# Kernel optimization log

Hardware: AMD Instinct MI355X
Metric: run time of the kernel (lower is better)

The kernel has to match this reference:

```python
import math
import jax, jax.numpy as jnp
import numpy as np

B, T, D, N = 4, 2048, 1024, 4096  # d_neuron = 4*d_model


def setup_inputs() -> dict:
    key = jax.random.key(0)
    ks = jax.random.split(key, 8)
    s_d = 1.0 / math.sqrt(D)
    s_n = 1.0 / math.sqrt(N)
    return {
        "x": jax.random.normal(ks[0], (B, T, D), jnp.float32),
        "state": jnp.zeros((B, N), jnp.float32),
        "W_main": jax.random.normal(ks[1], (D, N), jnp.float32) * s_d,
        "W_gate": jax.random.normal(ks[2], (D, N), jnp.float32) * s_d,
        "W_mod": jax.random.normal(ks[3], (D, N), jnp.float32) * s_d,
        "W_delta": jax.random.normal(ks[4], (D, N), jnp.float32) * s_d,
        "b_delta": jnp.full((N,), -3.0, jnp.float32),
        "W_out": jax.random.normal(ks[5], (N, D), jnp.float32) * s_n,
        "A_log": jnp.linspace(math.log(0.001), math.log(0.1), N).astype(jnp.float32),
        "sw_logit": jnp.zeros((N,), jnp.float32),  # inv_sigmoid(0.5)
    }


def reference(x, state, W_main, W_gate, W_mod, W_delta, b_delta, W_out, A_log, sw_logit):
    raw = jnp.einsum("btd,dn->btn", x, W_main)            # [B,T,N]
    gate = jax.nn.sigmoid(jnp.einsum("btd,dn->btn", x, W_gate))
    mod = jnp.tanh(jnp.einsum("btd,dn->btn", x, W_mod))
    delta = jax.nn.softplus(jnp.einsum("btd,dn->btn", x, W_delta) + b_delta)
    A = -jnp.exp(A_log)                                    # [N]
    decay = jnp.exp(delta * A)                             # [B,T,N]
    update = (1.0 - decay) * gate * jnp.tanh(raw)

    # linear recurrence h_t = decay_t * h_{t-1} + update_t via associative scan
    def combine(c, n):
        a1, b1 = c
        a2, b2 = n
        return a1 * a2, a2 * b1 + b2

    a_cum, b_cum = jax.lax.associative_scan(combine, (decay, update), axis=1)
    all_states = a_cum * state[:, None, :] + b_cum         # [B,T,N]
    final_state = all_states[:, -1]

    sw = jax.nn.sigmoid(sw_logit)
    mixed = (1.0 - sw) * jax.nn.gelu(raw, approximate=False) + sw * all_states
    output = mixed * (1.0 + mod)                           # dropout=0 (eval)
    output = jnp.einsum("btn,nd->btd", output, W_out)
    return output, final_state
```

## Files before the change

### kernel.cpp

```cpp
#include <hip/hip_runtime.h>
#include <math.h>
#include <stdint.h>

#define BB  4
#define TT  2048
#define DD  1024
#define NNq 4096
#define BT  (BB*TT)
#define NCH 16
#define TCH (TT/NCH)

typedef _Float16 f16;
typedef __attribute__((ext_vector_type(8))) _Float16 half8;
typedef __attribute__((ext_vector_type(4))) float f32x4;

__device__ __forceinline__ float sigmoid_f(float x){ return 1.f/(1.f+__expf(-x)); }
__device__ __forceinline__ float tanh_f(float x){
  float cx = fminf(fmaxf(x,-15.f),15.f);
  float e  = __expf(2.f*cx);
  return (e-1.f)/(e+1.f);
}
__device__ __forceinline__ float softplus_f(float x){
  return (x>15.f)? x : __logf(1.f+__expf(x));
}

__global__ __launch_bounds__(256) void cast_f16_k(const float* __restrict__ src,
                                                  f16* __restrict__ dst){
  size_t i = ((size_t)blockIdx.x*256 + threadIdx.x)*4;
  float4 v = *(const float4*)(src + i);
  union { f16 h[4]; uint2 u; } o;
  o.h[0]=(f16)v.x; o.h[1]=(f16)v.y; o.h[2]=(f16)v.z; o.h[3]=(f16)v.w;
  *(uint2*)(dst + i) = o.u;
}

__global__ __launch_bounds__(256) void transpose_cast_k(const float* __restrict__ src,
                                                        f16* __restrict__ dst,
                                                        int R, int C){
  __shared__ float tile[32][33];
  int c0 = blockIdx.x*32, r0 = blockIdx.y*32;
  int tx = threadIdx.x, ty = threadIdx.y;
  #pragma unroll
  for (int i=0;i<4;i++){ int r = ty + i*8; tile[r][tx] = src[(size_t)(r0+r)*C + c0+tx]; }
  __syncthreads();
  #pragma unroll
  for (int i=0;i<4;i++){ int c = ty + i*8; dst[(size_t)(c0+c)*R + r0+tx] = (f16)tile[tx][c]; }
}

template<int OUT_F32>
__global__ __launch_bounds__(256)
void gemm_bt(const f16* __restrict__ A, int lda,
             const f16* __restrict__ Bt, int ldb,
             void* __restrict__ Cout, int ldc, int K)
{
  __shared__ f16 lsA[128*64];
  __shared__ f16 lsB[128*64];
  const int tid  = threadIdx.x;
  const int lane = tid & 63;
  const int wave = tid >> 6;
  const int wm = wave >> 1, wn = wave & 1;
  const int m0 = blockIdx.y * 128;
  const int n0 = blockIdx.x * 128;

  const f16* Ag = A  + (size_t)m0 * lda;
  const f16* Bg = Bt + (size_t)n0 * ldb;

  f32x4 acc[4][4] = {};

  for (int k0 = 0; k0 < K; k0 += 64) {
    half8 ra[4], rb[4];
    #pragma unroll
    for (int i = 0; i < 4; i++) {
      const int j   = i*256 + tid;
      const int row = j >> 3;
      const int ce  = (j & 7) * 8;
      ra[i] = *(const half8*)(Ag + (size_t)row*lda + k0 + ce);
      rb[i] = *(const half8*)(Bg + (size_t)row*ldb + k0 + ce);
    }
    __syncthreads();
    #pragma unroll
    for (int i = 0; i < 4; i++) {
      const int j = i*256 + tid;
      *(half8*)&lsA[j*8] = ra[i];
      *(half8*)&lsB[j*8] = rb[i];
    }
    __syncthreads();
    #pragma unroll
    for (int ks = 0; ks < 2; ks++) {
      const int kk = ks*32 + (lane>>4)*8;
      half8 af[4], bfr[4];
      #pragma unroll
      for (int mi=0; mi<4; mi++)
        af[mi] = *(const half8*)&lsA[(wm*64 + mi*16 + (lane&15))*64 + kk];
      #pragma unroll
      for (int ni=0; ni<4; ni++)
        bfr[ni] = *(const half8*)&lsB[(wn*64 + ni*16 + (lane&15))*64 + kk];
      #pragma unroll
      for (int mi=0; mi<4; mi++)
        #pragma unroll
        for (int ni=0; ni<4; ni++)
          acc[mi][ni] = __builtin_amdgcn_mfma_f32_16x16x32_f16(af[mi], bfr[ni], acc[mi][ni], 0, 0, 0);
    }
  }

  const int crow = m0 + wm*64 + (lane>>4)*4;
  const int ccol = n0 + wn*64 + (lane&15);
  #pragma unroll
  for (int mi=0; mi<4; mi++)
    #pragma unroll
    for (int ni=0; ni<4; ni++)
      #pragma unroll
      for (int r=0; r<4; r++) {
        size_t idx = (size_t)(crow + mi*16 + r) * ldc + (ccol + ni*16);
        if (OUT_F32) ((float*)Cout)[idx] = acc[mi][ni][r];
        else         ((f16*)Cout)[idx]   = (f16)acc[mi][ni][r];
      }
}

__global__ __launch_bounds__(256) void scan_agg_k(
    const f16* __restrict__ zg, const f16* __restrict__ zr, const f16* __restrict__ zd,
    const float* __restrict__ Alog, const float* __restrict__ bdelta,
    float* __restrict__ AggA, float* __restrict__ AggB, int NC)
{
  const int nb = NC >> 8;
  const int bx = blockIdx.x;
  const int nl = (bx % nb)*256 + threadIdx.x;
  const int c  = (bx / nb) % NCH;
  const int b  = bx / (nb*NCH);
  const float An = -__expf(Alog[nl]);
  const float bd = bdelta[nl];
  float pA = 1.f, pB = 0.f;
  const size_t rbase = (size_t)(b*TT + c*TCH);
  #pragma unroll 4
  for (int t=0; t<TCH; ++t) {
    size_t rr = rbase + t;
    float g  = (float)zg[rr*NC  + nl];
    float r  = (float)zr[rr*NNq + nl];
    float dz = (float)zd[rr*NC  + nl] + bd;
    float d  = __expf(An * softplus_f(dz));
    float u  = (1.f-d) * sigmoid_f(g) * tanh_f(r);
    pA *= d;
    pB = fmaf(d, pB, u);
  }
  size_t o = ((size_t)(b*NCH + c))*NNq + nl;
  AggA[o] = pA;
  AggB[o] = pB;
}

__global__ __launch_bounds__(256) void scan_mid_k(
    const float* __restrict__ AggA, const float* __restrict__ AggB,
    const float* __restrict__ state0, float* __restrict__ sIn,
    float* __restrict__ fstate, int NC)
{
  int gi = blockIdx.x*256 + threadIdx.x;
  int b  = gi / NC, nl = gi % NC;
  float s = state0[(size_t)b*NNq + nl];
  #pragma unroll
  for (int c=0; c<NCH; ++c) {
    size_t o = ((size_t)(b*NCH + c))*NNq + nl;
    sIn[o] = s;
    s = fmaf(AggA[o], s, AggB[o]);
  }
  fstate[(size_t)b*NNq + nl] = s;
}

__global__ __launch_bounds__(256) void scan_apply_k(
    const f16* zr, const f16* __restrict__ zg, const f16* __restrict__ zm,
    const f16* __restrict__ zd,
    const float* __restrict__ Alog, const float* __restrict__ bdelta,
    const float* __restrict__ swl, const float* __restrict__ sIn,
    f16* P, int NC)
{
  const int nb = NC >> 8;
  const int bx = blockIdx.x;
  const int nl = (bx % nb)*256 + threadIdx.x;
  const int c  = (bx / nb) % NCH;
  const int b  = bx / (nb*NCH);
  const float An = -__expf(Alog[nl]);
  const float bd = bdelta[nl];
  const float sw = sigmoid_f(swl[nl]);
  float s = sIn[((size_t)(b*NCH + c))*NNq + nl];
  const size_t rbase = (size_t)(b*TT + c*TCH);
  for (int t=0; t<TCH; ++t) {
    size_t rr = rbase + t;
    float r  = (float)zr[rr*NNq + nl];
    float g  = (float)zg[rr*NC  + nl];
    float m  = (float)zm[rr*NC  + nl];
    float dz = (float)zd[rr*NC  + nl] + bd;
    float d  = __expf(An * softplus_f(dz));
    float u  = (1.f-d) * sigmoid_f(g) * tanh_f(r);
    s = fmaf(d, s, u);
    float gel = 0.5f*r*(1.f+erff(r*0.70710678118654752f));
    float mod = tanh_f(m);
    float op  = ((1.f-sw)*gel + sw*s)*(1.f+mod);
    P[rr*NNq + nl] = (f16)op;
  }
}

extern "C" void kernel_launch(void* const* d_in, const int* in_sizes, int n_in,
                              void* d_out, int out_size, void* d_ws, size_t ws_size,
                              hipStream_t stream)
{
  const float* x      = (const float*)d_in[0];
  const float* state0 = (const float*)d_in[1];
  const float* Wmain  = (const float*)d_in[2];
  const float* Wgate  = (const float*)d_in[3];
  const float* Wmod   = (const float*)d_in[4];
  const float* Wdelta = (const float*)d_in[5];
  const float* bdelta = (const float*)d_in[6];
  const float* Wout   = (const float*)d_in[7];
  const float* Alog   = (const float*)d_in[8];
  const float* swl    = (const float*)d_in[9];

  auto al = [](size_t v)->size_t { return (v + 255) & ~(size_t)255; };
  const size_t sz_xb  = al((size_t)BT*DD*2);
  const size_t sz_wt  = al((size_t)NNq*DD*2);
  const size_t sz_wto = al((size_t)DD*NNq*2);
  const size_t sz_P   = al((size_t)BT*NNq*2);
  const size_t sz_agg = al((size_t)BB*NCH*NNq*4);
  const size_t fixed  = sz_xb + 4*sz_wt + sz_wto + sz_P + 3*sz_agg;

  int NCC = 16;
  {
    const int cand[5] = {1,2,4,8,16};
    for (int i=0;i<5;i++){
      size_t zchunk = al((size_t)BT*(NNq/cand[i])*2);
      if (fixed + 3*zchunk <= ws_size) { NCC = cand[i]; break; }
    }
  }
  const int NC = NNq / NCC;
  const size_t sz_z = al((size_t)BT*NC*2);

  char* ws = (char*)d_ws;
  size_t off = 0;
  auto alloc = [&](size_t bytes)->void* { void* p = ws + off; off += bytes; return p; };
  f16*   xb   = (f16*)alloc(sz_xb);
  f16*   wt0  = (f16*)alloc(sz_wt);
  f16*   wt1  = (f16*)alloc(sz_wt);
  f16*   wt2  = (f16*)alloc(sz_wt);
  f16*   wt3  = (f16*)alloc(sz_wt);
  f16*   wto  = (f16*)alloc(sz_wto);
  f16*   P    = (f16*)alloc(sz_P);
  float* AggA = (float*)alloc(sz_agg);
  float* AggB = (float*)alloc(sz_agg);
  float* sIn  = (float*)alloc(sz_agg);
  f16*   z1   = (f16*)alloc(sz_z);
  f16*   z2   = (f16*)alloc(sz_z);
  f16*   z3   = (f16*)alloc(sz_z);

  float* fstate = (float*)d_out + (size_t)BT*DD;

  cast_f16_k<<<(BT*DD)/1024, 256, 0, stream>>>(x, xb);
  transpose_cast_k<<<dim3(NNq/32, DD/32), dim3(32,8), 0, stream>>>(Wmain,  wt0, DD, NNq);
  transpose_cast_k<<<dim3(NNq/32, DD/32), dim3(32,8), 0, stream>>>(Wgate,  wt1, DD, NNq);
  transpose_cast_k<<<dim3(NNq/32, DD/32), dim3(32,8), 0, stream>>>(Wmod,   wt2, DD, NNq);
  transpose_cast_k<<<dim3(NNq/32, DD/32), dim3(32,8), 0, stream>>>(Wdelta, wt3, DD, NNq);
  transpose_cast_k<<<dim3(DD/32, NNq/32), dim3(32,8), 0, stream>>>(Wout,   wto, NNq, DD);

  const dim3 gz(NC/128, BT/128);
  for (int cc = 0; cc < NCC; ++cc) {
    const int n0 = cc * NC;
    gemm_bt<0><<<gz, 256, 0, stream>>>(xb, DD, wt0 + (size_t)n0*DD, DD, P + n0, NNq, DD);
    gemm_bt<0><<<gz, 256, 0, stream>>>(xb, DD, wt1 + (size_t)n0*DD, DD, z1, NC, DD);
    gemm_bt<0><<<gz, 256, 0, stream>>>(xb, DD, wt2 + (size_t)n0*DD, DD, z2, NC, DD);
    gemm_bt<0><<<gz, 256, 0, stream>>>(xb, DD, wt3 + (size_t)n0*DD, DD, z3, NC, DD);
    scan_agg_k<<<BB*NCH*(NC/256), 256, 0, stream>>>(z1, P + n0, z3,
        Alog + n0, bdelta + n0, AggA + n0, AggB + n0, NC);
    scan_mid_k<<<(BB*NC)/256, 256, 0, stream>>>(AggA + n0, AggB + n0,
        state0 + n0, sIn + n0, fstate + n0, NC);
    scan_apply_k<<<BB*NCH*(NC/256), 256, 0, stream>>>(P + n0, z1, z2, z3,
        Alog + n0, bdelta + n0, swl + n0, sIn + n0, P + n0, NC);
  }

  gemm_bt<1><<<dim3(DD/128, BT/128), 256, 0, stream>>>(P, NNq, wto, NNq, d_out, DD, NNq);
}
```

Baseline: 967.5 us.

## Use direct global-to-LDS loads, XCD-aware tile remap, vectorized scans, more chunks

The GEMM now stages tiles with global_load_lds, which writes straight into shared memory instead of going through registers, and remaps workgroup IDs so neighbouring tiles land on the same XCD for better L2 reuse. The scan aggregate and apply kernels get vectorized variants that have each thread handle 2 or 4 neurons with packed f16 loads and stores. The number of time chunks doubles to raise scan parallelism. The trade-off is that the GEMM loses its register prefetch overlap, since the load now sits between two barriers, and the remap assumes the workgroup count is divisible by 8.

```diff
diff --git a/kernel.cpp b/kernel.cpp
--- a/kernel.cpp
+++ b/kernel.cpp
@@ -7,11 +7,13 @@
 #define DD  1024
 #define NNq 4096
 #define BT  (BB*TT)
-#define NCH 16
+#define NCH 32
 #define TCH (TT/NCH)
 
 typedef _Float16 f16;
 typedef __attribute__((ext_vector_type(8))) _Float16 half8;
+typedef __attribute__((ext_vector_type(4))) _Float16 half4;
+typedef __attribute__((ext_vector_type(2))) _Float16 half2v;
 typedef __attribute__((ext_vector_type(4))) float f32x4;
 
 __device__ __forceinline__ float sigmoid_f(float x){ return 1.f/(1.f+__expf(-x)); }
@@ -22,6 +24,13 @@
 }
 __device__ __forceinline__ float softplus_f(float x){
   return (x>15.f)? x : __logf(1.f+__expf(x));
+}
+
+__device__ __forceinline__ void gld_lds16(const void* g, void* l){
+  __builtin_amdgcn_global_load_lds(
+      (const __attribute__((address_space(1))) void*)(uintptr_t)g,
+      (__attribute__((address_space(3))) void*)(uintptr_t)l,
+      16, 0, 0);
 }
 
 __global__ __launch_bounds__(256) void cast_f16_k(const float* __restrict__ src,
@@ -58,8 +67,14 @@
   const int lane = tid & 63;
   const int wave = tid >> 6;
   const int wm = wave >> 1, wn = wave & 1;
-  const int m0 = blockIdx.y * 128;
-  const int n0 = blockIdx.x * 128;
+
+  const int gx   = gridDim.x;
+  const int nwg  = gx * gridDim.y;
+  const int orig = blockIdx.y * gx + blockIdx.x;
+  const int cpx  = nwg >> 3;
+  const int lgc  = (orig & 7) * cpx + (orig >> 3);
+  const int m0   = (lgc / gx) * 128;
+  const int n0   = (lgc % gx) * 128;
 
   const f16* Ag = A  + (size_t)m0 * lda;
   const f16* Bg = Bt + (size_t)n0 * ldb;
@@ -67,21 +82,14 @@
   f32x4 acc[4][4] = {};
 
   for (int k0 = 0; k0 < K; k0 += 64) {
-    half8 ra[4], rb[4];
+    __syncthreads();
     #pragma unroll
     for (int i = 0; i < 4; i++) {
       const int j   = i*256 + tid;
       const int row = j >> 3;
       const int ce  = (j & 7) * 8;
-      ra[i] = *(const half8*)(Ag + (size_t)row*lda + k0 + ce);
-      rb[i] = *(const half8*)(Bg + (size_t)row*ldb + k0 + ce);
-    }
-    __syncthreads();
-    #pragma unroll
-    for (int i = 0; i < 4; i++) {
-      const int j = i*256 + tid;
-      *(half8*)&lsA[j*8] = ra[i];
-      *(half8*)&lsB[j*8] = rb[i];
+      gld_lds16(Ag + (size_t)row*lda + k0 + ce, &lsA[j*8]);
+      gld_lds16(Bg + (size_t)row*ldb + k0 + ce, &lsB[j*8]);
     }
     __syncthreads();
     #pragma unroll
@@ -116,6 +124,46 @@
       }
 }
 
+template<int VEC>
+__global__ __launch_bounds__(256) void scan_agg_v(
+    const f16* __restrict__ zg, const f16* __restrict__ zr, const f16* __restrict__ zd,
+    const float* __restrict__ Alog, const float* __restrict__ bdelta,
+    float* __restrict__ AggA, float* __restrict__ AggB, int NC)
+{
+  typedef __attribute__((ext_vector_type(VEC))) _Float16 hv;
+  const int nb = NC / (256*VEC);
+  const int bx = blockIdx.x;
+  const int nl = ((bx % nb)*256 + threadIdx.x)*VEC;
+  const int c  = (bx / nb) % NCH;
+  const int b  = bx / (nb*NCH);
+  float An[VEC], bd[VEC], pA[VEC], pB[VEC];
+  #pragma unroll
+  for (int v=0;v<VEC;v++){
+    An[v] = -__expf(Alog[nl+v]); bd[v] = bdelta[nl+v]; pA[v]=1.f; pB[v]=0.f;
+  }
+  const size_t rbase = (size_t)(b*TT + c*TCH);
+  #pragma unroll 4
+  for (int t=0; t<TCH; ++t) {
+    size_t rr = rbase + t;
+    hv hg = *(const hv*)(zg + rr*NC + nl);
+    hv hr = *(const hv*)(zr + rr*(size_t)NNq + nl);
+    hv hd = *(const hv*)(zd + rr*NC + nl);
+    #pragma unroll
+    for (int v=0;v<VEC;v++){
+      float g  = (float)hg[v];
+      float r  = (float)hr[v];
+      float dz = (float)hd[v] + bd[v];
+      float d  = __expf(An[v] * softplus_f(dz));
+      float u  = (1.f-d) * sigmoid_f(g) * tanh_f(r);
+      pA[v] *= d;
+      pB[v] = fmaf(d, pB[v], u);
+    }
+  }
+  size_t o = ((size_t)(b*NCH + c))*NNq + nl;
+  #pragma unroll
+  for (int v=0;v<VEC;v++){ AggA[o+v]=pA[v]; AggB[o+v]=pB[v]; }
+}
+
 __global__ __launch_bounds__(256) void scan_agg_k(
     const f16* __restrict__ zg, const f16* __restrict__ zr, const f16* __restrict__ zd,
     const float* __restrict__ Alog, const float* __restrict__ bdelta,
@@ -134,7 +182,7 @@
   for (int t=0; t<TCH; ++t) {
     size_t rr = rbase + t;
     float g  = (float)zg[rr*NC  + nl];
-    float r  = (float)zr[rr*NNq + nl];
+    float r  = (float)zr[rr*(size_t)NNq + nl];
     float dz = (float)zd[rr*NC  + nl] + bd;
     float d  = __expf(An * softplus_f(dz));
     float u  = (1.f-d) * sigmoid_f(g) * tanh_f(r);
@@ -161,6 +209,52 @@
     s = fmaf(AggA[o], s, AggB[o]);
   }
   fstate[(size_t)b*NNq + nl] = s;
+}
+
+template<int VEC>
+__global__ __launch_bounds__(256) void scan_apply_v(
+    const f16* zr, const f16* __restrict__ zg, const f16* __restrict__ zm,
+    const f16* __restrict__ zd,
+    const float* __restrict__ Alog, const float* __restrict__ bdelta,
+    const float* __restrict__ swl, const float* __restrict__ sIn,
+    f16* P, int NC)
+{
+  typedef __attribute__((ext_vector_type(VEC))) _Float16 hv;
+  const int nb = NC / (256*VEC);
+  const int bx = blockIdx.x;
+  const int nl = ((bx % nb)*256 + threadIdx.x)*VEC;
+  const int c  = (bx / nb) % NCH;
+  const int b  = bx / (nb*NCH);
+  float An[VEC], bd[VEC], sw[VEC], s[VEC];
+  #pragma unroll
+  for (int v=0;v<VEC;v++){
+    An[v] = -__expf(Alog[nl+v]); bd[v] = bdelta[nl+v];
+    sw[v] = sigmoid_f(swl[nl+v]);
+    s[v]  = sIn[((size_t)(b*NCH + c))*NNq + nl + v];
+  }
+  const size_t rbase = (size_t)(b*TT + c*TCH);
+  for (int t=0; t<TCH; ++t) {
+    size_t rr = rbase + t;
+    hv hr = *(const hv*)(zr + rr*(size_t)NNq + nl);
+    hv hg = *(const hv*)(zg + rr*NC + nl);
+    hv hm = *(const hv*)(zm + rr*NC + nl);
+    hv hd = *(const hv*)(zd + rr*NC + nl);
+    hv ho;
+    #pragma unroll
+    for (int v=0;v<VEC;v++){
+      float r  = (float)hr[v];
+      float g  = (float)hg[v];
+      float m  = (float)hm[v];
+      float dz = (float)hd[v] + bd[v];
+      float d  = __expf(An[v] * softplus_f(dz));
+      float u  = (1.f-d) * sigmoid_f(g) * tanh_f(r);
+      s[v] = fmaf(d, s[v], u);
+      float gel = 0.5f*r*(1.f+erff(r*0.70710678118654752f));
+      float mod = tanh_f(m);
+      ho[v] = (f16)(((1.f-sw[v])*gel + sw[v]*s[v])*(1.f+mod));
+    }
+    *(hv*)(P + rr*(size_t)NNq + nl) = ho;
+  }
 }
 
 __global__ __launch_bounds__(256) void scan_apply_k(
@@ -182,7 +276,7 @@
   const size_t rbase = (size_t)(b*TT + c*TCH);
   for (int t=0; t<TCH; ++t) {
     size_t rr = rbase + t;
-    float r  = (float)zr[rr*NNq + nl];
+    float r  = (float)zr[rr*(size_t)NNq + nl];
     float g  = (float)zg[rr*NC  + nl];
     float m  = (float)zm[rr*NC  + nl];
     float dz = (float)zd[rr*NC  + nl] + bd;
@@ -191,8 +285,7 @@
     s = fmaf(d, s, u);
     float gel = 0.5f*r*(1.f+erff(r*0.70710678118654752f));
     float mod = tanh_f(m);
-    float op  = ((1.f-sw)*gel + sw*s)*(1.f+mod);
-    P[rr*NNq + nl] = (f16)op;
+    P[rr*(size_t)NNq + nl] = (f16)(((1.f-sw)*gel + sw*s)*(1.f+mod));
   }
 }
 
@@ -256,6 +349,7 @@
   transpose_cast_k<<<dim3(NNq/32, DD/32), dim3(32,8), 0, stream>>>(Wdelta, wt3, DD, NNq);
   transpose_cast_k<<<dim3(DD/32, NNq/32), dim3(32,8), 0, stream>>>(Wout,   wto, NNq, DD);
 
+  const int VEC = (NC >= 2048) ? 4 : ((NC >= 512) ? 2 : 1);
   const dim3 gz(NC/128, BT/128);
   for (int cc = 0; cc < NCC; ++cc) {
     const int n0 = cc * NC;
@@ -263,12 +357,31 @@
     gemm_bt<0><<<gz, 256, 0, stream>>>(xb, DD, wt1 + (size_t)n0*DD, DD, z1, NC, DD);
     gemm_bt<0><<<gz, 256, 0, stream>>>(xb, DD, wt2 + (size_t)n0*DD, DD, z2, NC, DD);
     gemm_bt<0><<<gz, 256, 0, stream>>>(xb, DD, wt3 + (size_t)n0*DD, DD, z3, NC, DD);
-    scan_agg_k<<<BB*NCH*(NC/256), 256, 0, stream>>>(z1, P + n0, z3,
-        Alog + n0, bdelta + n0, AggA + n0, AggB + n0, NC);
+
+    if (VEC == 4) {
+      scan_agg_v<4><<<BB*NCH*(NC/1024), 256, 0, stream>>>(z1, P + n0, z3,
+          Alog + n0, bdelta + n0, AggA + n0, AggB + n0, NC);
+    } else if (VEC == 2) {
+      scan_agg_v<2><<<BB*NCH*(NC/512), 256, 0, stream>>>(z1, P + n0, z3,
+          Alog + n0, bdelta + n0, AggA + n0, AggB + n0, NC);
+    } else {
+      scan_agg_k<<<BB*NCH*(NC/256), 256, 0, stream>>>(z1, P + n0, z3,
+          Alog + n0, bdelta + n0, AggA + n0, AggB + n0, NC);
+    }
+
     scan_mid_k<<<(BB*NC)/256, 256, 0, stream>>>(AggA + n0, AggB + n0,
         state0 + n0, sIn + n0, fstate + n0, NC);
-    scan_apply_k<<<BB*NCH*(NC/256), 256, 0, stream>>>(P + n0, z1, z2, z3,
-        Alog + n0, bdelta + n0, swl + n0, sIn + n0, P + n0, NC);
+
+    if (VEC == 4) {
+      scan_apply_v<4><<<BB*NCH*(NC/1024), 256, 0, stream>>>(P + n0, z1, z2, z3,
+          Alog + n0, bdelta + n0, swl + n0, sIn + n0, P + n0, NC);
+    } else if (VEC == 2) {
+      scan_apply_v<2><<<BB*NCH*(NC/512), 256, 0, stream>>>(P + n0, z1, z2, z3,
+          Alog + n0, bdelta + n0, swl + n0, sIn + n0, P + n0, NC);
+    } else {
+      scan_apply_k<<<BB*NCH*(NC/256), 256, 0, stream>>>(P + n0, z1, z2, z3,
+          Alog + n0, bdelta + n0, swl + n0, sIn + n0, P + n0, NC);
+    }
   }
 
   gemm_bt<1><<<dim3(DD/128, BT/128), 256, 0, stream>>>(P, NNq, wto, NNq, d_out, DD, NNq);
```

After: 1.005 ms. 1.04x slower.
